# Kernel optimization log

Measured on AMD Instinct MI355X. Metric: run time of the kernel, lower is better.

## Reference

```python
import jax, jax.numpy as jnp
import numpy as np

NUM_GRAPHS = 64
EPS = 1e-6


def setup_inputs() -> dict:
    key = jax.random.key(0)
    ks = jax.random.split(key, 16)
    S, B, IN, H, N, P_IN, P_OUT = 256, 64, 3, 128, 1_000_000, 8, 32
    src = jax.random.normal(ks[0], (S, B, IN), dtype=jnp.float32)
    src_len = jnp.maximum(jax.random.randint(ks[1], (B,), 0, S + 1), 1).astype(jnp.int32)
    node_x = jax.random.normal(ks[2], (N, H), dtype=jnp.float32)
    # w is a 0/1 node validity mask in the original (float)
    node_w = (jax.random.uniform(ks[3], (N,)) < 0.9).astype(jnp.float32)
    graph_ids = jnp.sort(jax.random.randint(ks[4], (N,), 0, NUM_GRAPHS)).astype(jnp.int32)
    pro_features = jax.random.normal(ks[5], (B, P_IN), dtype=jnp.float32)
    s_in = 1.0 / np.sqrt(IN)
    s_h = 1.0 / np.sqrt(H)
    s_p = 1.0 / np.sqrt(P_IN)
    s_c = 1.0 / np.sqrt(H + P_OUT)
    W_in = jax.random.uniform(ks[6], (IN, H), minval=-s_in, maxval=s_in)
    b_in = jax.random.uniform(ks[7], (H,), minval=-s_in, maxval=s_in)
    W_pred = jax.random.uniform(ks[8], (H, 1), minval=-s_h, maxval=s_h)
    b_pred = jax.random.uniform(ks[9], (1,), minval=-s_h, maxval=s_h)
    W_extra = jax.random.uniform(ks[10], (P_IN, P_OUT), minval=-s_p, maxval=s_p)
    b_extra = jax.random.uniform(ks[11], (P_OUT,), minval=-s_p, maxval=s_p)
    W_hid = jax.random.uniform(ks[12], (P_OUT + H, H), minval=-s_c, maxval=s_c)
    b_hid = jax.random.uniform(ks[13], (H,), minval=-s_c, maxval=s_c)
    return {"src": src, "src_len": src_len, "node_x": node_x, "node_w": node_w,
            "graph_ids": graph_ids, "pro_features": pro_features,
            "W_in": W_in, "b_in": b_in, "W_pred": W_pred, "b_pred": b_pred,
            "W_extra": W_extra, "b_extra": b_extra, "W_hid": W_hid, "b_hid": b_hid}


def mask_graph_log_softmax(lg, w, graph_ids):
    # lg: [N], w: [N], graph_ids: [N] sorted segment ids -> per-graph masked softmax, then log
    maxes = jax.ops.segment_max(lg, graph_ids, num_segments=NUM_GRAPHS)
    x_exp = jnp.exp(lg - maxes[graph_ids]) * w
    x_sum = jax.ops.segment_sum(x_exp, graph_ids, num_segments=NUM_GRAPHS)
    pred = x_exp / (x_sum[graph_ids] + EPS)
    return jnp.log(jnp.clip(pred, EPS, 1.0))


def reference(src, src_len, node_x, node_w, graph_ids, pro_features,
              W_in, b_in, W_pred, b_pred, W_extra, b_extra, W_hid, b_hid):
    S, B = src.shape[0], src.shape[1]
    # mask2d[i, t] = 1 for t < src_len[i]
    mask2d = (jnp.arange(S)[None, :] < src_len[:, None]).astype(src.dtype)  # [B, S]
    h = jnp.tanh(0.0) + src @ W_in + b_in  # [S, B, H]  (fc_in; transformer treated as identity)
    # zero out padded timesteps, then mean over dim 0 (torch.mean divides by S)
    outputs = h * mask2d.T[:, :, None]  # [S, B, H]
    hidden = jnp.mean(outputs, axis=0, keepdims=True)  # [1, B, H]
    # graph segment softmax on node scores
    lg = (node_x @ W_pred + b_pred)[:, 0]  # [N]
    lg_out = mask_graph_log_softmax(lg, node_w, graph_ids)[:, None]  # [N, 1]
    # pro feature fusion
    extra_emb = jnp.tanh(pro_features @ W_extra + b_extra)[None]  # [1, B, P_OUT]
    hidden = jnp.tanh(jnp.concatenate((extra_emb, hidden), axis=2) @ W_hid + b_hid)  # [1, B, H]
    return outputs, hidden, lg_out
```

## Files before the change

kernel.cpp:

```cpp
#include <hip/hip_runtime.h>

#define S_DIM 256
#define B_DIM 64
#define IN_DIM 3
#define H_DIM 128
#define N_NODES 1000000
#define NM1 (N_NODES - 1)
#define P_INF 8
#define P_OUTF 32
#define NUM_GRAPHS 64
#define EPSF 1e-6f

#define OUT_OUTPUTS 0
#define OUT_HIDDEN (S_DIM * B_DIM * H_DIM)
#define OUT_LG (OUT_HIDDEN + B_DIM * H_DIM)

#define NBLK 2048
#define RPB 489
#define RPW 123
#define SG_SLOTS 6

#define WS_HIDPART 0
#define WS_TBLV (8 * B_DIM * H_DIM)
#define WS_TBLG (WS_TBLV + NBLK * SG_SLOTS)

__global__ void __launch_bounds__(256)
main_kernel(const float* __restrict__ src, const int* __restrict__ src_len,
            const float* __restrict__ W_in, const float* __restrict__ b_in,
            const float* __restrict__ node_x, const float* __restrict__ W_pred,
            const float* __restrict__ b_pred, const float* __restrict__ node_w,
            const int* __restrict__ gids,
            float* __restrict__ outputs, float* __restrict__ hid_partial,
            float* __restrict__ lg, float* __restrict__ tblV, int* __restrict__ tblG) {
    __shared__ float sg[SG_SLOTS];
    const int tid = threadIdx.x;
    const int blk = blockIdx.x;
    if (tid < SG_SLOTS) sg[tid] = 0.0f;

    if (blk < 256) {
        int b = blk & 63;
        int chunk = blk >> 6;
        int h = tid & 127;
        int shalf = tid >> 7;
        float w0 = W_in[h], w1 = W_in[H_DIM + h], w2 = W_in[2 * H_DIM + h];
        float bi = b_in[h];
        int len = src_len[b];
        float facc = 0.0f;
        int s0 = chunk * 64 + shalf * 32;
        for (int s = s0; s < s0 + 32; ++s) {
            const float* sp = src + ((size_t)s * B_DIM + b) * IN_DIM;
            float v = fmaf(sp[0], w0, fmaf(sp[1], w1, fmaf(sp[2], w2, bi)));
            v = (s < len) ? v : 0.0f;
            outputs[((size_t)s * B_DIM + b) * H_DIM + h] = v;
            facc += v;
        }
        hid_partial[((size_t)(chunk * 2 + shalf) * B_DIM + b) * H_DIM + h] = facc;
    }
    __syncthreads();

    const int start = blk * RPB;
    const int bend = min(start + RPB, N_NODES);
    const int gfirst = gids[min(start, NM1)];
    const int wid = tid >> 6;
    const int lane = tid & 63;
    const int p = lane & 7;
    const int rloc = lane >> 3;
    const int wstart = start + wid * RPW;
    const int wend = min(wstart + RPW, bend);

    float4 wch0 = ((const float4*)W_pred)[p];
    float4 wch1 = ((const float4*)W_pred)[p + 8];
    float4 wch2 = ((const float4*)W_pred)[p + 16];
    float4 wch3 = ((const float4*)W_pred)[p + 24];
    const float bp = b_pred[0];

    int curg = -1;
    float acc = 0.0f;

    float4 cx0, cx1, cx2, cx3;
    float cwv = 0.0f;
    int cgv = 0;

#define LOADG(R0, X0, X1, X2, X3, WV, GV)                                   \
    {                                                                        \
        int sidx = min((R0) + p, NM1);                                       \
        WV = node_w[sidx];                                                   \
        GV = gids[sidx];                                                     \
        int xrow = min((R0) + rloc, NM1);                                    \
        const float4* xb = (const float4*)(node_x + (size_t)xrow * H_DIM);   \
        X0 = xb[p];                                                          \
        X1 = xb[p + 8];                                                      \
        X2 = xb[p + 16];                                                     \
        X3 = xb[p + 24];                                                     \
    }

    if (wstart < wend) {
        LOADG(wstart, cx0, cx1, cx2, cx3, cwv, cgv);
    }

    for (int r0 = wstart; r0 < wend; r0 += 8) {
        float4 nx0, nx1, nx2, nx3;
        float nwv = 0.0f;
        int ngv = 0;
        const int nr0 = r0 + 8;
        if (nr0 < wend) {
            LOADG(nr0, nx0, nx1, nx2, nx3, nwv, ngv);
        }
        float s = cx0.x * wch0.x + cx0.y * wch0.y + cx0.z * wch0.z + cx0.w * wch0.w;
        s += cx1.x * wch1.x + cx1.y * wch1.y + cx1.z * wch1.z + cx1.w * wch1.w;
        s += cx2.x * wch2.x + cx2.y * wch2.y + cx2.z * wch2.z + cx2.w * wch2.w;
        s += cx3.x * wch3.x + cx3.y * wch3.y + cx3.z * wch3.z + cx3.w * wch3.w;
        s += __shfl_xor(s, 1);
        s += __shfl_xor(s, 2);
        s += __shfl_xor(s, 4);
        float rowsum = __shfl(s, p * 8);
        int myrow = r0 + p;
        if (lane < 8 && myrow < wend) {
            float score = rowsum + bp;
            lg[myrow] = score;
            float xe = __expf(score) * cwv;
            if (cgv != curg) {
                if (curg >= 0) atomicAdd(&sg[min(curg - gfirst, SG_SLOTS - 1)], acc);
                curg = cgv;
                acc = 0.0f;
            }
            acc += xe;
        }
        cx0 = nx0; cx1 = nx1; cx2 = nx2; cx3 = nx3;
        cwv = nwv; cgv = ngv;
    }
#undef LOADG
    if (curg >= 0) atomicAdd(&sg[min(curg - gfirst, SG_SLOTS - 1)], acc);
    __syncthreads();
    if (tid < SG_SLOTS) tblV[blk * SG_SLOTS + tid] = sg[tid];
    if (tid == 0) tblG[blk] = gfirst;
}

#define LGOUT_BLOCKS 977

__global__ void __launch_bounds__(256)
finish_kernel(const float* __restrict__ tblV, const int* __restrict__ tblG,
              float* __restrict__ lg, const int* __restrict__ gids,
              const float* __restrict__ node_w,
              const float* __restrict__ pro, const float* __restrict__ W_extra,
              const float* __restrict__ b_extra, const float* __restrict__ W_hid,
              const float* __restrict__ b_hid, const float* __restrict__ hid_partial,
              float* __restrict__ hidden_out) {
    const int tid = threadIdx.x;
    const int blk = blockIdx.x;

    if (blk >= LGOUT_BLOCKS) {
        int b = blk - LGOUT_BLOCKS;
        __shared__ float sh[P_OUTF + H_DIM];
        if (tid < P_OUTF) {
            float a = b_extra[tid];
            #pragma unroll
            for (int k = 0; k < P_INF; ++k) a += pro[b * P_INF + k] * W_extra[k * P_OUTF + tid];
            sh[tid] = tanhf(a);
        }
        if (tid < H_DIM) {
            float m = 0.0f;
            #pragma unroll
            for (int c = 0; c < 8; ++c) m += hid_partial[((size_t)c * B_DIM + b) * H_DIM + tid];
            sh[P_OUTF + tid] = m * (1.0f / S_DIM);
        }
        __syncthreads();
        if (tid < H_DIM) {
            float a = b_hid[tid];
            #pragma unroll 8
            for (int k = 0; k < P_OUTF + H_DIM; ++k) a += sh[k] * W_hid[k * H_DIM + tid];
            hidden_out[(size_t)b * H_DIM + tid] = tanhf(a);
        }
        return;
    }

    __shared__ float gsum[NUM_GRAPHS];
    if (tid < NUM_GRAPHS) gsum[tid] = 0.0f;
    __syncthreads();
    {
        int cg2 = -1;
        float a = 0.0f;
        for (int b = tid * (NBLK / 256); b < (tid + 1) * (NBLK / 256); ++b) {
            int gf = tblG[b];
            #pragma unroll
            for (int slot = 0; slot < SG_SLOTS; ++slot) {
                float v = tblV[b * SG_SLOTS + slot];
                if (v != 0.0f) {
                    int g = min(gf + slot, NUM_GRAPHS - 1);
                    if (g != cg2) {
                        if (cg2 >= 0) atomicAdd(&gsum[cg2], a);
                        cg2 = g;
                        a = 0.0f;
                    }
                    a += v;
                }
            }
        }
        if (cg2 >= 0) atomicAdd(&gsum[cg2], a);
    }
    __syncthreads();

    int n4 = blk * 256 + tid;
    if (n4 >= N_NODES / 4) return;
    float4 l = ((const float4*)lg)[n4];
    float4 w = ((const float4*)node_w)[n4];
    int4 g = ((const int4*)gids)[n4];
    float4 r;
    r.x = __logf(fminf(fmaxf(__expf(l.x) * w.x / (gsum[g.x] + EPSF), EPSF), 1.0f));
    r.y = __logf(fminf(fmaxf(__expf(l.y) * w.y / (gsum[g.y] + EPSF), EPSF), 1.0f));
    r.z = __logf(fminf(fmaxf(__expf(l.z) * w.z / (gsum[g.z] + EPSF), EPSF), 1.0f));
    r.w = __logf(fminf(fmaxf(__expf(l.w) * w.w / (gsum[g.w] + EPSF), EPSF), 1.0f));
    ((float4*)lg)[n4] = r;
}

extern "C" void kernel_launch(void* const* d_in, const int* in_sizes, int n_in,
                              void* d_out, int out_size, void* d_ws, size_t ws_size,
                              hipStream_t stream) {
    const float* src      = (const float*)d_in[0];
    const int*   src_len  = (const int*)d_in[1];
    const float* node_x   = (const float*)d_in[2];
    const float* node_w   = (const float*)d_in[3];
    const int*   gids     = (const int*)d_in[4];
    const float* pro      = (const float*)d_in[5];
    const float* W_in     = (const float*)d_in[6];
    const float* b_in     = (const float*)d_in[7];
    const float* W_pred   = (const float*)d_in[8];
    const float* b_pred   = (const float*)d_in[9];
    const float* W_extra  = (const float*)d_in[10];
    const float* b_extra  = (const float*)d_in[11];
    const float* W_hid    = (const float*)d_in[12];
    const float* b_hid    = (const float*)d_in[13];

    float* out = (float*)d_out;
    float* outputs = out + OUT_OUTPUTS;
    float* hidden  = out + OUT_HIDDEN;
    float* lg      = out + OUT_LG;

    float* ws = (float*)d_ws;
    float* hid_partial = ws + WS_HIDPART;
    float* tblV = ws + WS_TBLV;
    int*   tblG = (int*)(ws + WS_TBLG);

    main_kernel<<<NBLK, 256, 0, stream>>>(src, src_len, W_in, b_in,
                                          node_x, W_pred, b_pred, node_w, gids,
                                          outputs, hid_partial, lg, tblV, tblG);

    finish_kernel<<<LGOUT_BLOCKS + B_DIM, 256, 0, stream>>>(tblV, tblG, lg, gids, node_w,
                                                            pro, W_extra, b_extra, W_hid,
                                                            b_hid, hid_partial, hidden);
}
```

Baseline: 140.4 us.

## Use 512-thread blocks with warp-interleaved row striding for node scoring

Halves the grid to 1024 blocks of 512 threads, each covering about 977 node rows. The eight warps in a block now take interleaved 8-row groups with a 64-row stride, instead of each warp owning a contiguous chunk. The fc_in part splits each 64-step chunk into four quarters, so there are 16 hidden partial sums, and the finish kernel sums over 16. The aim is better coalescing and load balance across warps for the large node_x stream. The cost is larger blocks, which can limit occupancy, and more shared-memory atomic traffic when group boundaries are crossed.

New measurement: 122.0 us. 1.15x faster.

```diff
diff --git a/kernel.cpp b/kernel.cpp
--- a/kernel.cpp
+++ b/kernel.cpp
@@ -15,16 +15,17 @@
 #define OUT_HIDDEN (S_DIM * B_DIM * H_DIM)
 #define OUT_LG (OUT_HIDDEN + B_DIM * H_DIM)
 
-#define NBLK 2048
-#define RPB 489
-#define RPW 123
+#define NBLK 1024
+#define TPB 512
+#define RPB 977
+#define GSTEP 64
 #define SG_SLOTS 6
 
 #define WS_HIDPART 0
-#define WS_TBLV (8 * B_DIM * H_DIM)
+#define WS_TBLV (16 * B_DIM * H_DIM)
 #define WS_TBLG (WS_TBLV + NBLK * SG_SLOTS)
 
-__global__ void __launch_bounds__(256)
+__global__ void __launch_bounds__(TPB)
 main_kernel(const float* __restrict__ src, const int* __restrict__ src_len,
             const float* __restrict__ W_in, const float* __restrict__ b_in,
             const float* __restrict__ node_x, const float* __restrict__ W_pred,
@@ -41,32 +42,30 @@
         int b = blk & 63;
         int chunk = blk >> 6;
         int h = tid & 127;
-        int shalf = tid >> 7;
+        int sq = tid >> 7;
         float w0 = W_in[h], w1 = W_in[H_DIM + h], w2 = W_in[2 * H_DIM + h];
         float bi = b_in[h];
         int len = src_len[b];
         float facc = 0.0f;
-        int s0 = chunk * 64 + shalf * 32;
-        for (int s = s0; s < s0 + 32; ++s) {
+        int s0 = chunk * 64 + sq * 16;
+        for (int s = s0; s < s0 + 16; ++s) {
             const float* sp = src + ((size_t)s * B_DIM + b) * IN_DIM;
             float v = fmaf(sp[0], w0, fmaf(sp[1], w1, fmaf(sp[2], w2, bi)));
             v = (s < len) ? v : 0.0f;
             outputs[((size_t)s * B_DIM + b) * H_DIM + h] = v;
             facc += v;
         }
-        hid_partial[((size_t)(chunk * 2 + shalf) * B_DIM + b) * H_DIM + h] = facc;
+        hid_partial[((size_t)(chunk * 4 + sq) * B_DIM + b) * H_DIM + h] = facc;
     }
     __syncthreads();
 
     const int start = blk * RPB;
     const int bend = min(start + RPB, N_NODES);
     const int gfirst = gids[min(start, NM1)];
-    const int wid = tid >> 6;
+    const int w = tid >> 6;
     const int lane = tid & 63;
     const int p = lane & 7;
     const int rloc = lane >> 3;
-    const int wstart = start + wid * RPW;
-    const int wend = min(wstart + RPW, bend);
 
     float4 wch0 = ((const float4*)W_pred)[p];
     float4 wch1 = ((const float4*)W_pred)[p + 8];
@@ -94,16 +93,16 @@
         X3 = xb[p + 24];                                                     \
     }
 
-    if (wstart < wend) {
-        LOADG(wstart, cx0, cx1, cx2, cx3, cwv, cgv);
-    }
-
-    for (int r0 = wstart; r0 < wend; r0 += 8) {
+    int r0 = start + w * 8;
+    if (r0 < bend) {
+        LOADG(r0, cx0, cx1, cx2, cx3, cwv, cgv);
+    }
+    while (r0 < bend) {
+        const int nr0 = r0 + GSTEP;
         float4 nx0, nx1, nx2, nx3;
         float nwv = 0.0f;
         int ngv = 0;
-        const int nr0 = r0 + 8;
-        if (nr0 < wend) {
+        if (nr0 < bend) {
             LOADG(nr0, nx0, nx1, nx2, nx3, nwv, ngv);
         }
         float s = cx0.x * wch0.x + cx0.y * wch0.y + cx0.z * wch0.z + cx0.w * wch0.w;
@@ -115,7 +114,7 @@
         s += __shfl_xor(s, 4);
         float rowsum = __shfl(s, p * 8);
         int myrow = r0 + p;
-        if (lane < 8 && myrow < wend) {
+        if (lane < 8 && myrow < bend) {
             float score = rowsum + bp;
             lg[myrow] = score;
             float xe = __expf(score) * cwv;
@@ -128,6 +127,7 @@
         }
         cx0 = nx0; cx1 = nx1; cx2 = nx2; cx3 = nx3;
         cwv = nwv; cgv = ngv;
+        r0 = nr0;
     }
 #undef LOADG
     if (curg >= 0) atomicAdd(&sg[min(curg - gfirst, SG_SLOTS - 1)], acc);
@@ -161,7 +161,7 @@
         if (tid < H_DIM) {
             float m = 0.0f;
             #pragma unroll
-            for (int c = 0; c < 8; ++c) m += hid_partial[((size_t)c * B_DIM + b) * H_DIM + tid];
+            for (int c = 0; c < 16; ++c) m += hid_partial[((size_t)c * B_DIM + b) * H_DIM + tid];
             sh[P_OUTF + tid] = m * (1.0f / S_DIM);
         }
         __syncthreads();
@@ -241,7 +241,7 @@
     float* tblV = ws + WS_TBLV;
     int*   tblG = (int*)(ws + WS_TBLG);
 
-    main_kernel<<<NBLK, 256, 0, stream>>>(src, src_len, W_in, b_in,
+    main_kernel<<<NBLK, TPB, 0, stream>>>(src, src_len, W_in, b_in,
                                           node_x, W_pred, b_pred, node_w, gids,
                                           outputs, hid_partial, lg, tblV, tblG);
 
```
